# Performance work log

Hardware: AMD Instinct MI355X
Metric: run time of the kernel (lower is better)

The kernel has to match this reference:

```python
import jax, jax.numpy as jnp
import numpy as np

N = 50000   # nodes
E = 800000  # edges
F = 128     # input features
H = 128     # hidden channels
G = 64      # graphs in batch
C = 10      # classes
L_HID = 3   # residual hidden GCN blocks
EPS = 1e-5  # BatchNorm eps


def setup_inputs() -> dict:
    key = jax.random.key(0)
    ks = jax.random.split(key, 10)
    sc = lambda k, s: (jax.random.normal(k, s, jnp.float32) * 0.05)
    x = jax.random.normal(ks[0], (N, F), jnp.float32)
    edge_index = jax.random.randint(ks[1], (2, E), 0, N, dtype=jnp.int32)
    batch = jnp.sort(jax.random.randint(ks[2], (N,), 0, G, dtype=jnp.int32))
    return {
        "x": x, "edge_index": edge_index, "batch": batch,
        # initial GCN block
        "W0": sc(ks[3], (F, H)), "b0": jnp.zeros(H, jnp.float32),
        "g0": jnp.ones(H, jnp.float32), "be0": jnp.zeros(H, jnp.float32),
        # 3 residual GCN blocks (stacked)
        "Wh": sc(ks[4], (L_HID, H, H)), "bh": jnp.zeros((L_HID, H), jnp.float32),
        "gh": jnp.ones((L_HID, H), jnp.float32), "beh": jnp.zeros((L_HID, H), jnp.float32),
        "Rh": sc(ks[5], (L_HID, H, H)),  # residual Linear (no bias)
        # MLP head: Linear(H,H)+ReLU, Linear(H,C)
        "mW1": sc(ks[6], (H, H)), "mb1": jnp.zeros(H, jnp.float32),
        "mW2": sc(ks[7], (H, C)), "mb2": jnp.zeros(C, jnp.float32),
    }


def _gcn_norm(edge_index, n):
    # add self-loops + symmetric normalization, as in PyG GCNConv
    loop = jnp.arange(n, dtype=edge_index.dtype)
    src = jnp.concatenate([edge_index[0], loop])
    dst = jnp.concatenate([edge_index[1], loop])
    deg = jax.ops.segment_sum(jnp.ones_like(dst, jnp.float32), dst, num_segments=n)
    dinv = jnp.where(deg > 0, jax.lax.rsqrt(deg), 0.0)
    coef = dinv[src] * dinv[dst]  # [E+N]
    return src, dst, coef


def _gcn_conv(x, W, b, src, dst, coef, n):
    h = x @ W                                   # [N, H] linear first (PyG order)
    msg = h[src] * coef[:, None]                # gather + normalize  [E+N, H]
    agg = jax.ops.segment_sum(msg, dst, num_segments=n)  # scatter-add [N, H]
    return agg + b


def _bn_relu(h, gamma, beta):
    # BatchNorm1d in eval mode with running_mean=0, running_var=1
    inv = jax.lax.rsqrt(jnp.asarray(1.0 + EPS, h.dtype))
    return jax.nn.relu(h * inv * gamma + beta)  # dropout is identity in eval


def reference(x, edge_index, batch, W0, b0, g0, be0, Wh, bh, gh, beh, Rh, mW1, mb1, mW2, mb2):
    n = x.shape[0]
    src, dst, coef = _gcn_norm(edge_index, n)
    # initial block (no residual)
    h = _bn_relu(_gcn_conv(x, W0, b0, src, dst, coef, n), g0, be0)
    # residual hidden blocks
    for i in range(Wh.shape[0]):
        c = _gcn_conv(h, Wh[i], bh[i], src, dst, coef, n) + h @ Rh[i]
        h = _bn_relu(c, gh[i], beh[i])
    # global max pool over graphs in the batch
    pooled = jax.ops.segment_max(h, batch, num_segments=G)  # [G, H]
    # MLP head
    z = jax.nn.relu(pooled @ mW1 + mb1)
    return z @ mW2 + mb2  # [G, C]
```

## Files before the change

### kernel.cpp

```cpp
#include <hip/hip_runtime.h>
#include <cstdint>
#include <cstddef>

#define NN 50000
#define NE 800000
#define NEPAD (NE + 3 * NN)
#define HID 128
#define NGRAPH 64
#define NCLASS 10
#define LHID 3
#define NREP 8

#define ROWBLK 3125
#define ROWBLK_PAD 3128
#define GEMM_GRID 782
#define FILL_GRID 3125
#define FRONT_DEG 3125
#define FRONT_B 56
#define FRONT_GRID (FRONT_DEG + FRONT_B)

static constexpr float BN_INV = 0.9999950000374996f;

typedef __attribute__((ext_vector_type(8))) __bf16 bf16x8;
typedef __attribute__((ext_vector_type(4))) float floatx4;


__device__ __forceinline__ unsigned int f32_to_bf16_rne(float f) {
    unsigned int u = __float_as_uint(f);
    return (u + 0x7FFFu + ((u >> 16) & 1u)) >> 16;
}
__device__ __forceinline__ float bf16_to_f32(unsigned int h) {
    return __uint_as_float(h << 16);
}
__device__ __forceinline__ void split2(float a, float b, unsigned int& hi,
                                       unsigned int& lo) {
    unsigned int h0 = f32_to_bf16_rne(a), h1 = f32_to_bf16_rne(b);
    unsigned int l0 = f32_to_bf16_rne(a - bf16_to_f32(h0));
    unsigned int l1 = f32_to_bf16_rne(b - bf16_to_f32(h1));
    hi = h0 | (h1 << 16);
    lo = l0 | (l1 << 16);
}


__global__ void k_front(const float* __restrict__ W0, const float* __restrict__ Wh,
                        const float* __restrict__ Rh, unsigned short* __restrict__ bH,
                        unsigned short* __restrict__ bL,
                        const int* __restrict__ ei, int* __restrict__ deg8,
                        int* __restrict__ eslot) {
    const int b = blockIdx.x;
    const int tid = threadIdx.x;
    if (b < FRONT_DEG) {
        int e = b * 256 + tid;
        int d = ei[NE + e];
        int rep = e & (NREP - 1);
        eslot[e] = atomicAdd(&deg8[rep * NN + d], 1);
    } else {
        int cb = b - FRONT_DEG;
        int mat = cb >> 3;
        const float* src = (mat == 0) ? W0
                         : (mat <= 3) ? (Wh + (size_t)(mat - 1) * 16384)
                                      : (Rh + (size_t)(mat - 4) * 16384);
        int u = (cb & 7) * 256 + tid;
        int lane = u & 63;
        int blk = u >> 6;
        int kblk = blk & 3;
        int nb = blk >> 2;
        int n = nb * 16 + (lane & 15);
        int k = kblk * 32 + (lane >> 4) * 8;
        union { unsigned int i[4]; uint4 v; } H, L;
#pragma unroll
        for (int j = 0; j < 4; ++j) {
            float a = src[(size_t)(k + 2 * j) * 128 + n];
            float c = src[(size_t)(k + 2 * j + 1) * 128 + n];
            split2(a, c, H.i[j], L.i[j]);
        }
        size_t base = (size_t)mat * 16384 + (size_t)u * 8;
        *(uint4*)&bH[base] = H.v;
        *(uint4*)&bL[base] = L.v;
    }
}


__global__ void k_scan1(const int* __restrict__ deg8, int* __restrict__ degT,
                        int* __restrict__ degOff, float* __restrict__ dinv,
                        int* __restrict__ bsum) {
    __shared__ int s[256];
    int i = blockIdx.x * 256 + threadIdx.x;
    int dsum = 0;
    if (i < NN) {
        int off[NREP];
#pragma unroll
        for (int r = 0; r < NREP; ++r) {
            off[r] = dsum;
            dsum += deg8[r * NN + i];
        }
#pragma unroll
        for (int r = 0; r < NREP; ++r) degOff[i * NREP + r] = off[r];
        degT[i] = dsum;
        dinv[i] = rsqrtf((float)(dsum + 1));
    }
    s[threadIdx.x] = (dsum + 3) & ~3;
    __syncthreads();
    for (int o = 128; o > 0; o >>= 1) {
        if (threadIdx.x < o) s[threadIdx.x] += s[threadIdx.x + o];
        __syncthreads();
    }
    if (threadIdx.x == 0) bsum[blockIdx.x] = s[0];
}


__global__ void k_scan3(const int* __restrict__ degT, const int* __restrict__ bsum,
                        int* __restrict__ rowptr, int* __restrict__ col,
                        float* __restrict__ cfv) {
    __shared__ int s[256];
    __shared__ int offS;
    const int bid = blockIdx.x;
    s[threadIdx.x] = (threadIdx.x < bid) ? bsum[threadIdx.x] : 0;
    __syncthreads();
    for (int o = 128; o > 0; o >>= 1) {
        if (threadIdx.x < o) s[threadIdx.x] += s[threadIdx.x + o];
        __syncthreads();
    }
    if (threadIdx.x == 0) offS = s[0];
    __syncthreads();
    const int off = offS;
    __syncthreads();
    int i = bid * 256 + threadIdx.x;
    int d = (i < NN) ? degT[i] : 0;
    int v = (d + 3) & ~3;
    s[threadIdx.x] = v;
    __syncthreads();
    for (int o = 1; o < 256; o <<= 1) {
        int tv = (threadIdx.x >= o) ? s[threadIdx.x - o] : 0;
        __syncthreads();
        s[threadIdx.x] += tv;
        __syncthreads();
    }
    if (i < NN) {
        int rp = off + s[threadIdx.x] - v;
        rowptr[i] = rp;
        for (int p = rp + d; p < rp + v; ++p) { col[p] = 0; cfv[p] = 0.f; }
    }
}


template <int NB, bool FILL, bool XA>
__global__ __launch_bounds__(256, 3) void k_gemm_mfma(
    const float* __restrict__ X,
    const unsigned short* __restrict__ Ahi, const unsigned short* __restrict__ Alo,
    const unsigned short* __restrict__ B1hi, const unsigned short* __restrict__ B1lo,
    const unsigned short* __restrict__ B2hi, const unsigned short* __restrict__ B2lo,
    float* __restrict__ C1, float* __restrict__ C2,
    const int* __restrict__ ei, const int* __restrict__ rowptr,
    const int* __restrict__ eslot, const int* __restrict__ degOff,
    const float* __restrict__ dinv, int* __restrict__ col,
    float* __restrict__ cfv) {
    if (FILL && blockIdx.x >= GEMM_GRID) {
        int e = (blockIdx.x - GEMM_GRID) * 256 + threadIdx.x;
        int s = ei[e];
        int d = ei[NE + e];
        int rep = e & (NREP - 1);
        int p = rowptr[d] + degOff[d * NREP + rep] + eslot[e];
        col[p] = s;
        cfv[p] = dinv[s];
        return;
    }
    const int tid = threadIdx.x;
    const int wave = tid >> 6;
    const int lane = tid & 63;
    const int wm = wave & 1;
    const int wn = wave >> 1;
    const int rb0 = blockIdx.x * 4;

    floatx4 acc1[2][4], acc2[2][4];
    floatx4 zero = {0.f, 0.f, 0.f, 0.f};
#pragma unroll
    for (int i = 0; i < 2; ++i)
#pragma unroll
        for (int j = 0; j < 4; ++j) { acc1[i][j] = zero; if (NB == 2) acc2[i][j] = zero; }

#pragma unroll
    for (int kc = 0; kc < 4; ++kc) {
        bf16x8 aH[2], aL[2], bH[4], bL[4];
        if (XA) {
#pragma unroll
            for (int t = 0; t < 2; ++t) {
                int m = (rb0 + wm * 2 + t) * 16 + (lane & 15);
                if (m >= NN) m = NN - 1;
                const float4* p =
                    (const float4*)&X[(size_t)m * 128 + kc * 32 + (lane >> 4) * 8];
                float4 v0 = p[0];
                float4 v1 = p[1];
                float vals[8] = {v0.x, v0.y, v0.z, v0.w, v1.x, v1.y, v1.z, v1.w};
                union { unsigned int i[4]; bf16x8 v; } H, L;
#pragma unroll
                for (int j = 0; j < 4; ++j)
                    split2(vals[2 * j], vals[2 * j + 1], H.i[j], L.i[j]);
                aH[t] = H.v;
                aL[t] = L.v;
            }
        } else {
#pragma unroll
            for (int t = 0; t < 2; ++t) {
                size_t u = ((size_t)(rb0 + wm * 2 + t) * 4 + kc) * 512 + lane * 8;
                aH[t] = *(const bf16x8*)(Ahi + u);
                aL[t] = *(const bf16x8*)(Alo + u);
            }
        }
#pragma unroll
        for (int t = 0; t < 4; ++t)
            bH[t] = *(const bf16x8*)(B1hi + ((size_t)(wn * 4 + t) * 4 + kc) * 512 +
                                     lane * 8);
#pragma unroll
        for (int tm = 0; tm < 2; ++tm)
#pragma unroll
            for (int tn = 0; tn < 4; ++tn)
                acc1[tm][tn] = __builtin_amdgcn_mfma_f32_16x16x32_bf16(
                    aH[tm], bH[tn], acc1[tm][tn], 0, 0, 0);
#pragma unroll
        for (int t = 0; t < 4; ++t)
            bL[t] = *(const bf16x8*)(B1lo + ((size_t)(wn * 4 + t) * 4 + kc) * 512 +
                                     lane * 8);
#pragma unroll
        for (int tm = 0; tm < 2; ++tm)
#pragma unroll
            for (int tn = 0; tn < 4; ++tn)
                acc1[tm][tn] = __builtin_amdgcn_mfma_f32_16x16x32_bf16(
                    aH[tm], bL[tn], acc1[tm][tn], 0, 0, 0);
#pragma unroll
        for (int tm = 0; tm < 2; ++tm)
#pragma unroll
            for (int tn = 0; tn < 4; ++tn)
                acc1[tm][tn] = __builtin_amdgcn_mfma_f32_16x16x32_bf16(
                    aL[tm], bH[tn], acc1[tm][tn], 0, 0, 0);
        if (NB == 2) {
#pragma unroll
            for (int t = 0; t < 4; ++t)
                bH[t] = *(const bf16x8*)(B2hi + ((size_t)(wn * 4 + t) * 4 + kc) * 512 +
                                         lane * 8);
#pragma unroll
            for (int tm = 0; tm < 2; ++tm)
#pragma unroll
                for (int tn = 0; tn < 4; ++tn)
                    acc2[tm][tn] = __builtin_amdgcn_mfma_f32_16x16x32_bf16(
                        aH[tm], bH[tn], acc2[tm][tn], 0, 0, 0);
#pragma unroll
            for (int tm = 0; tm < 2; ++tm)
#pragma unroll
                for (int tn = 0; tn < 4; ++tn)
                    acc2[tm][tn] = __builtin_amdgcn_mfma_f32_16x16x32_bf16(
                        aL[tm], bH[tn], acc2[tm][tn], 0, 0, 0);
#pragma unroll
            for (int t = 0; t < 4; ++t)
                bL[t] = *(const bf16x8*)(B2lo + ((size_t)(wn * 4 + t) * 4 + kc) * 512 +
                                         lane * 8);
#pragma unroll
            for (int tm = 0; tm < 2; ++tm)
#pragma unroll
                for (int tn = 0; tn < 4; ++tn)
                    acc2[tm][tn] = __builtin_amdgcn_mfma_f32_16x16x32_bf16(
                        aH[tm], bL[tn], acc2[tm][tn], 0, 0, 0);
        }
    }

    const int quad = lane >> 4;
    const int col0 = lane & 15;
    const int rowBase = blockIdx.x * 64 + wm * 32;
#pragma unroll
    for (int tm = 0; tm < 2; ++tm) {
#pragma unroll
        for (int tn = 0; tn < 4; ++tn) {
            int c = wn * 64 + tn * 16 + col0;
#pragma unroll
            for (int r = 0; r < 4; ++r) {
                int row = rowBase + tm * 16 + quad * 4 + r;
                if (row < NN) {
                    C1[(size_t)row * 128 + c] = acc1[tm][tn][r];
                    if (NB == 2) C2[(size_t)row * 128 + c] = acc2[tm][tn][r];
                }
            }
        }
    }
}


template <bool RES, bool LAST>
__global__ __launch_bounds__(1024, 8) void k_spmm(
    const float* __restrict__ t, const float* __restrict__ r,
    const int* __restrict__ rowptr, const int* __restrict__ degT,
    const int* __restrict__ col, const float* __restrict__ cfv,
    const float* __restrict__ dinv, const float* __restrict__ bias,
    const float* __restrict__ gamma, const float* __restrict__ beta,
    unsigned short* __restrict__ hHi, unsigned short* __restrict__ hLo,
    const int* __restrict__ batch, float* __restrict__ pooled) {
    __shared__ unsigned short shH[16][136];
    __shared__ unsigned short shL[16][136];
    __shared__ float shP[16][128];
    const int tid = threadIdx.x;
    const int lane = tid & 63;
    const int h = lane >> 5;
    const int f4 = lane & 31;
    const int wv = __builtin_amdgcn_readfirstlane(tid >> 6);
    const int node = blockIdx.x * 16 + wv;

    const int start = __builtin_amdgcn_readfirstlane(rowptr[node]);
    const int cnt4 = __builtin_amdgcn_readfirstlane((degT[node] + 3) >> 2);

    float4 acc = {0.f, 0.f, 0.f, 0.f};
#pragma unroll 4
    for (int q = 0; q < cnt4; ++q) {
        const int4 cs = *(const int4*)(col + start + q * 4);
        const float4 wvv = *(const float4*)(cfv + start + q * 4);
        const int rowA = h ? cs.y : cs.x;
        const int rowB = h ? cs.w : cs.z;
        const float wA = h ? wvv.y : wvv.x;
        const float wB = h ? wvv.w : wvv.z;
        const float4 vA = *(const float4*)&t[(size_t)rowA * 128 + f4 * 4];
        const float4 vB = *(const float4*)&t[(size_t)rowB * 128 + f4 * 4];
        acc.x = fmaf(wA, vA.x, acc.x); acc.y = fmaf(wA, vA.y, acc.y);
        acc.z = fmaf(wA, vA.z, acc.z); acc.w = fmaf(wA, vA.w, acc.w);
        acc.x = fmaf(wB, vB.x, acc.x); acc.y = fmaf(wB, vB.y, acc.y);
        acc.z = fmaf(wB, vB.z, acc.z); acc.w = fmaf(wB, vB.w, acc.w);
    }
    acc.x += __shfl_xor(acc.x, 32);
    acc.y += __shfl_xor(acc.y, 32);
    acc.z += __shfl_xor(acc.z, 32);
    acc.w += __shfl_xor(acc.w, 32);

    const int f0 = f4 * 4;
    float4 o;
    if (h == 0) {
        const float di = dinv[node];
        const float dii = di * di;
        const float4 tv = *(const float4*)&t[(size_t)node * 128 + f0];
        const float4 bv = *(const float4*)&bias[f0];
        const float4 gv = *(const float4*)&gamma[f0];
        const float4 ev = *(const float4*)&beta[f0];
        float4 cc;
        cc.x = di * acc.x + dii * tv.x + bv.x;
        cc.y = di * acc.y + dii * tv.y + bv.y;
        cc.z = di * acc.z + dii * tv.z + bv.z;
        cc.w = di * acc.w + dii * tv.w + bv.w;
        if (RES) {
            const float4 rv = *(const float4*)&r[(size_t)node * 128 + f0];
            cc.x += rv.x; cc.y += rv.y; cc.z += rv.z; cc.w += rv.w;
        }
        o.x = fmaxf(cc.x * (BN_INV * gv.x) + ev.x, 0.f);
        o.y = fmaxf(cc.y * (BN_INV * gv.y) + ev.y, 0.f);
        o.z = fmaxf(cc.z * (BN_INV * gv.z) + ev.z, 0.f);
        o.w = fmaxf(cc.w * (BN_INV * gv.w) + ev.w, 0.f);
    }

    if (LAST) {
        bool uni = (batch[blockIdx.x * 16] == batch[blockIdx.x * 16 + 15]);
        if (uni) {
            if (h == 0) *(float4*)&shP[wv][f0] = o;
            __syncthreads();
            if (wv == 0) {
                float a = shP[0][2 * lane], b = shP[0][2 * lane + 1];
#pragma unroll
                for (int w = 1; w < 16; ++w) {
                    a = fmaxf(a, shP[w][2 * lane]);
                    b = fmaxf(b, shP[w][2 * lane + 1]);
                }
                int g = batch[blockIdx.x * 16];
                atomicMax((unsigned int*)&pooled[g * 128 + 2 * lane],
                          __float_as_uint(a));
                atomicMax((unsigned int*)&pooled[g * 128 + 2 * lane + 1],
                          __float_as_uint(b));
            }
        } else if (h == 0) {
            int g = batch[node];
            atomicMax((unsigned int*)&pooled[g * 128 + f0], __float_as_uint(o.x));
            atomicMax((unsigned int*)&pooled[g * 128 + f0 + 1], __float_as_uint(o.y));
            atomicMax((unsigned int*)&pooled[g * 128 + f0 + 2], __float_as_uint(o.z));
            atomicMax((unsigned int*)&pooled[g * 128 + f0 + 3], __float_as_uint(o.w));
        }
        return;
    }

    if (h == 0) {
        unsigned int H0, L0, H1, L1;
        split2(o.x, o.y, H0, L0);
        split2(o.z, o.w, H1, L1);
        ((unsigned int*)&shH[wv][0])[f4 * 2] = H0;
        ((unsigned int*)&shH[wv][0])[f4 * 2 + 1] = H1;
        ((unsigned int*)&shL[wv][0])[f4 * 2] = L0;
        ((unsigned int*)&shL[wv][0])[f4 * 2 + 1] = L1;
    }
    __syncthreads();

    const int u = tid >> 6;
    const int l = tid & 63;
    const int m = l & 15;
    const int kg = l >> 4;
    if (u < 4) {
        uint4 H4 = *(const uint4*)&shH[m][u * 32 + kg * 8];
        ((uint4*)hHi)[((size_t)blockIdx.x * 4 + u) * 64 + l] = H4;
    } else if (u < 8) {
        int uu = u - 4;
        uint4 L4 = *(const uint4*)&shL[m][uu * 32 + kg * 8];
        ((uint4*)hLo)[((size_t)blockIdx.x * 4 + uu) * 64 + l] = L4;
    }
}


__global__ void k_head(const float* __restrict__ pooled, const float* __restrict__ mW1,
                       const float* __restrict__ mb1, const float* __restrict__ mW2,
                       const float* __restrict__ mb2, float* __restrict__ out) {
    __shared__ float p[128];
    __shared__ float z[128];
    int g = blockIdx.x;
    int j = threadIdx.x;
    p[j] = pooled[g * 128 + j];
    __syncthreads();
    float a = mb1[j];
#pragma unroll 8
    for (int k = 0; k < 128; ++k) a += p[k] * mW1[k * 128 + j];
    z[j] = fmaxf(a, 0.f);
    __syncthreads();
    if (j < NCLASS) {
        float o = mb2[j];
#pragma unroll 8
        for (int k = 0; k < 128; ++k) o += z[k] * mW2[k * NCLASS + j];
        out[g * NCLASS + j] = o;
    }
}


extern "C" void kernel_launch(void* const* d_in, const int* in_sizes, int n_in,
                              void* d_out, int out_size, void* d_ws, size_t ws_size,
                              hipStream_t stream) {
    const float* x   = (const float*)d_in[0];
    const int*   ei  = (const int*)d_in[1];
    const int* batch = (const int*)d_in[2];
    const float* W0  = (const float*)d_in[3];
    const float* b0  = (const float*)d_in[4];
    const float* g0  = (const float*)d_in[5];
    const float* be0 = (const float*)d_in[6];
    const float* Wh  = (const float*)d_in[7];
    const float* bh  = (const float*)d_in[8];
    const float* gh  = (const float*)d_in[9];
    const float* beh = (const float*)d_in[10];
    const float* Rh  = (const float*)d_in[11];
    const float* mW1 = (const float*)d_in[12];
    const float* mb1 = (const float*)d_in[13];
    const float* mW2 = (const float*)d_in[14];
    const float* mb2 = (const float*)d_in[15];
    float* out = (float*)d_out;

    char* ws = (char*)d_ws;
    size_t off = 0;
    auto alloc = [&](size_t bytes) -> void* {
        void* p = ws + off;
        off += (bytes + 255) & ~(size_t)255;
        return p;
    };
    int*   deg8   = (int*)alloc((size_t)NREP * NN * 4);
    float* pooled = (float*)alloc((size_t)NGRAPH * HID * 4);
    size_t zspan = (size_t)((char*)pooled - (char*)deg8) + (size_t)NGRAPH * HID * 4;
    int*   degT   = (int*)alloc((size_t)NN * 4);
    int*   degOff = (int*)alloc((size_t)NN * NREP * 4);
    int*   rowptr = (int*)alloc((size_t)NN * 4);
    float* dinv   = (float*)alloc((size_t)NN * 4);
    int*   bsum   = (int*)alloc(256 * 4);
    int*   eslot  = (int*)alloc((size_t)NE * 4);
    int*   col    = (int*)alloc((size_t)NEPAD * 4);
    float* cfv    = (float*)alloc((size_t)NEPAD * 4);
    float* t      = (float*)alloc((size_t)NN * HID * 4);
    float* rbuf   = (float*)alloc((size_t)NN * HID * 4);
    const size_t ASZ = (size_t)ROWBLK_PAD * 4 * 512;
    unsigned short* hH0 = (unsigned short*)alloc(ASZ * 2);
    unsigned short* hL0 = (unsigned short*)alloc(ASZ * 2);
    unsigned short* hH1 = (unsigned short*)alloc(ASZ * 2);
    unsigned short* hL1 = (unsigned short*)alloc(ASZ * 2);
    unsigned short* bH = (unsigned short*)alloc((size_t)7 * 16384 * 2);
    unsigned short* bL = (unsigned short*)alloc((size_t)7 * 16384 * 2);

    hipMemsetAsync(deg8, 0, zspan, stream);

    k_front<<<FRONT_GRID, 256, 0, stream>>>(W0, Wh, Rh, bH, bL, ei, deg8, eslot);
    k_scan1<<<(NN + 255) / 256, 256, 0, stream>>>(deg8, degT, degOff, dinv, bsum);
    k_scan3<<<(NN + 255) / 256, 256, 0, stream>>>(degT, bsum, rowptr, col, cfv);

    k_gemm_mfma<1, true, true><<<GEMM_GRID + FILL_GRID, 256, 0, stream>>>(
        x, nullptr, nullptr, bH, bL, nullptr, nullptr, t, nullptr,
        ei, rowptr, eslot, degOff, dinv, col, cfv);

    const int spmmGrid = NN / 16;
    k_spmm<false, false><<<spmmGrid, 1024, 0, stream>>>(
        t, nullptr, rowptr, degT, col, cfv, dinv, b0, g0, be0, hH0, hL0,
        nullptr, nullptr);

    unsigned short* hh[2] = {hH0, hH1};
    unsigned short* hl[2] = {hL0, hL1};
    int cur = 0;
    for (int i = 0; i < LHID; ++i) {
        unsigned short* ih = hh[cur];
        unsigned short* il = hl[cur];
        unsigned short* oh = hh[cur ^ 1];
        unsigned short* ol = hl[cur ^ 1];
        const unsigned short* w1H = bH + (size_t)(1 + i) * 16384;
        const unsigned short* w1L = bL + (size_t)(1 + i) * 16384;
        const unsigned short* w2H = bH + (size_t)(4 + i) * 16384;
        const unsigned short* w2L = bL + (size_t)(4 + i) * 16384;
        k_gemm_mfma<2, false, false><<<GEMM_GRID, 256, 0, stream>>>(
            nullptr, ih, il, w1H, w1L, w2H, w2L, t, rbuf,
            nullptr, nullptr, nullptr, nullptr, nullptr, nullptr, nullptr);
        if (i < LHID - 1)
            k_spmm<true, false><<<spmmGrid, 1024, 0, stream>>>(
                t, rbuf, rowptr, degT, col, cfv, dinv, bh + i * HID, gh + i * HID,
                beh + i * HID, oh, ol, nullptr, nullptr);
        else
            k_spmm<true, true><<<spmmGrid, 1024, 0, stream>>>(
                t, rbuf, rowptr, degT, col, cfv, dinv, bh + i * HID, gh + i * HID,
                beh + i * HID, nullptr, nullptr, batch, pooled);
        cur ^= 1;
    }

    k_head<<<NGRAPH, 128, 0, stream>>>(pooled, mW1, mb1, mW2, mb2, out);
}
```

Baseline: 502.2 us.

## Fuse next layer's dual GEMM into SpMM epilogue, removing separate GEMM launches

The SpMM kernel now multiplies its 16 freshly aggregated node rows (held in shared memory as bf16 hi/lo splits) by the next layer's W and residual R matrices using MFMA, and writes the fp32 t and r outputs directly. This removes the three standalone GEMM kernels and the write and re-read of the intermediate bf16 hidden state. It uses ping-pong t/r buffers instead. The cost is extra MFMA work and weight-fragment loads inside each SpMM block, with weights read from global memory per wave rather than staged.

```diff
diff --git a/kernel.cpp b/kernel.cpp
--- a/kernel.cpp
+++ b/kernel.cpp
@@ -291,7 +291,9 @@
     const int* __restrict__ col, const float* __restrict__ cfv,
     const float* __restrict__ dinv, const float* __restrict__ bias,
     const float* __restrict__ gamma, const float* __restrict__ beta,
-    unsigned short* __restrict__ hHi, unsigned short* __restrict__ hLo,
+    const unsigned short* __restrict__ w1H, const unsigned short* __restrict__ w1L,
+    const unsigned short* __restrict__ w2H, const unsigned short* __restrict__ w2L,
+    float* __restrict__ tOut, float* __restrict__ rOut,
     const int* __restrict__ batch, float* __restrict__ pooled) {
     __shared__ unsigned short shH[16][136];
     __shared__ unsigned short shL[16][136];
@@ -390,18 +392,30 @@
     }
     __syncthreads();
 
-    const int u = tid >> 6;
-    const int l = tid & 63;
-    const int m = l & 15;
-    const int kg = l >> 4;
-    if (u < 4) {
-        uint4 H4 = *(const uint4*)&shH[m][u * 32 + kg * 8];
-        ((uint4*)hHi)[((size_t)blockIdx.x * 4 + u) * 64 + l] = H4;
-    } else if (u < 8) {
-        int uu = u - 4;
-        uint4 L4 = *(const uint4*)&shL[m][uu * 32 + kg * 8];
-        ((uint4*)hLo)[((size_t)blockIdx.x * 4 + uu) * 64 + l] = L4;
-    }
+    const int w = tid >> 6;
+    const int mat = w >> 3;
+    const int nb = w & 7;
+    const unsigned short* BH = mat ? w2H : w1H;
+    const unsigned short* BL = mat ? w2L : w1L;
+    float* outp = mat ? rOut : tOut;
+    floatx4 accG = {0.f, 0.f, 0.f, 0.f};
+#pragma unroll
+    for (int kc = 0; kc < 4; ++kc) {
+        const int ao = kc * 32 + (lane >> 4) * 8;
+        bf16x8 aH = *(const bf16x8*)&shH[lane & 15][ao];
+        bf16x8 aL = *(const bf16x8*)&shL[lane & 15][ao];
+        bf16x8 bHv = *(const bf16x8*)(BH + ((size_t)nb * 4 + kc) * 512 + lane * 8);
+        bf16x8 bLv = *(const bf16x8*)(BL + ((size_t)nb * 4 + kc) * 512 + lane * 8);
+        accG = __builtin_amdgcn_mfma_f32_16x16x32_bf16(aH, bHv, accG, 0, 0, 0);
+        accG = __builtin_amdgcn_mfma_f32_16x16x32_bf16(aH, bLv, accG, 0, 0, 0);
+        accG = __builtin_amdgcn_mfma_f32_16x16x32_bf16(aL, bHv, accG, 0, 0, 0);
+    }
+    const int quad = lane >> 4;
+    const int c0 = nb * 16 + (lane & 15);
+    const int row0 = blockIdx.x * 16 + quad * 4;
+#pragma unroll
+    for (int rr = 0; rr < 4; ++rr)
+        outp[(size_t)(row0 + rr) * 128 + c0] = accG[rr];
 }
 
 
@@ -467,13 +481,10 @@
     int*   eslot  = (int*)alloc((size_t)NE * 4);
     int*   col    = (int*)alloc((size_t)NEPAD * 4);
     float* cfv    = (float*)alloc((size_t)NEPAD * 4);
-    float* t      = (float*)alloc((size_t)NN * HID * 4);
-    float* rbuf   = (float*)alloc((size_t)NN * HID * 4);
-    const size_t ASZ = (size_t)ROWBLK_PAD * 4 * 512;
-    unsigned short* hH0 = (unsigned short*)alloc(ASZ * 2);
-    unsigned short* hL0 = (unsigned short*)alloc(ASZ * 2);
-    unsigned short* hH1 = (unsigned short*)alloc(ASZ * 2);
-    unsigned short* hL1 = (unsigned short*)alloc(ASZ * 2);
+    float* tA     = (float*)alloc((size_t)NN * HID * 4);
+    float* tB     = (float*)alloc((size_t)NN * HID * 4);
+    float* rA     = (float*)alloc((size_t)NN * HID * 4);
+    float* rB     = (float*)alloc((size_t)NN * HID * 4);
     unsigned short* bH = (unsigned short*)alloc((size_t)7 * 16384 * 2);
     unsigned short* bL = (unsigned short*)alloc((size_t)7 * 16384 * 2);
 
@@ -484,39 +495,36 @@
     k_scan3<<<(NN + 255) / 256, 256, 0, stream>>>(degT, bsum, rowptr, col, cfv);
 
     k_gemm_mfma<1, true, true><<<GEMM_GRID + FILL_GRID, 256, 0, stream>>>(
-        x, nullptr, nullptr, bH, bL, nullptr, nullptr, t, nullptr,
+        x, nullptr, nullptr, bH, bL, nullptr, nullptr, tA, nullptr,
         ei, rowptr, eslot, degOff, dinv, col, cfv);
 
     const int spmmGrid = NN / 16;
+
     k_spmm<false, false><<<spmmGrid, 1024, 0, stream>>>(
-        t, nullptr, rowptr, degT, col, cfv, dinv, b0, g0, be0, hH0, hL0,
-        nullptr, nullptr);
-
-    unsigned short* hh[2] = {hH0, hH1};
-    unsigned short* hl[2] = {hL0, hL1};
-    int cur = 0;
-    for (int i = 0; i < LHID; ++i) {
-        unsigned short* ih = hh[cur];
-        unsigned short* il = hl[cur];
-        unsigned short* oh = hh[cur ^ 1];
-        unsigned short* ol = hl[cur ^ 1];
-        const unsigned short* w1H = bH + (size_t)(1 + i) * 16384;
-        const unsigned short* w1L = bL + (size_t)(1 + i) * 16384;
-        const unsigned short* w2H = bH + (size_t)(4 + i) * 16384;
-        const unsigned short* w2L = bL + (size_t)(4 + i) * 16384;
-        k_gemm_mfma<2, false, false><<<GEMM_GRID, 256, 0, stream>>>(
-            nullptr, ih, il, w1H, w1L, w2H, w2L, t, rbuf,
-            nullptr, nullptr, nullptr, nullptr, nullptr, nullptr, nullptr);
-        if (i < LHID - 1)
-            k_spmm<true, false><<<spmmGrid, 1024, 0, stream>>>(
-                t, rbuf, rowptr, degT, col, cfv, dinv, bh + i * HID, gh + i * HID,
-                beh + i * HID, oh, ol, nullptr, nullptr);
-        else
-            k_spmm<true, true><<<spmmGrid, 1024, 0, stream>>>(
-                t, rbuf, rowptr, degT, col, cfv, dinv, bh + i * HID, gh + i * HID,
-                beh + i * HID, nullptr, nullptr, batch, pooled);
-        cur ^= 1;
-    }
+        tA, nullptr, rowptr, degT, col, cfv, dinv, b0, g0, be0,
+        bH + (size_t)1 * 16384, bL + (size_t)1 * 16384,
+        bH + (size_t)4 * 16384, bL + (size_t)4 * 16384,
+        tB, rB, nullptr, nullptr);
+
+    k_spmm<true, false><<<spmmGrid, 1024, 0, stream>>>(
+        tB, rB, rowptr, degT, col, cfv, dinv, bh + 0 * HID, gh + 0 * HID,
+        beh + 0 * HID,
+        bH + (size_t)2 * 16384, bL + (size_t)2 * 16384,
+        bH + (size_t)5 * 16384, bL + (size_t)5 * 16384,
+        tA, rA, nullptr, nullptr);
+
+    k_spmm<true, false><<<spmmGrid, 1024, 0, stream>>>(
+        tA, rA, rowptr, degT, col, cfv, dinv, bh + 1 * HID, gh + 1 * HID,
+        beh + 1 * HID,
+        bH + (size_t)3 * 16384, bL + (size_t)3 * 16384,
+        bH + (size_t)6 * 16384, bL + (size_t)6 * 16384,
+        tB, rB, nullptr, nullptr);
+
+    k_spmm<true, true><<<spmmGrid, 1024, 0, stream>>>(
+        tB, rB, rowptr, degT, col, cfv, dinv, bh + 2 * HID, gh + 2 * HID,
+        beh + 2 * HID,
+        nullptr, nullptr, nullptr, nullptr,
+        nullptr, nullptr, batch, pooled);
 
     k_head<<<NGRAPH, 128, 0, stream>>>(pooled, mW1, mb1, mW2, mb2, out);
 }
```

After: 474.6 us. 1.06x faster.

## Slice feature matrix into 16-column panels and pack edge metadata for SpMM

Applied to the files above, without the earlier changes.

The GEMM now writes its output in eight column-sliced panels of 16 floats per node, and the SpMM grid is multiplied by 8 so each block aggregates one 16-feature slice. With 16 edges per wave in parallel, each gather is a 64-byte contiguous row piece. Edge column index and source degree are packed into one int, with the coefficient recomputed by rsqrt, which replaces the separate col and cfv arrays. The intent is to keep each slice's gather working set small enough to stay in cache. In exchange, metadata is re-read eight times and more blocks are launched. The hidden-state buffers are also reorganised: one h buffer with ping-ponged t and r buffers.

```diff
diff --git a/kernel.cpp b/kernel.cpp
--- a/kernel.cpp
+++ b/kernel.cpp
@@ -18,6 +18,9 @@
 #define FRONT_DEG 3125
 #define FRONT_B 56
 #define FRONT_GRID (FRONT_DEG + FRONT_B)
+
+#define SPMM_GRID (NN / 16 * 8)
+#define SLICE_STRIDE ((size_t)NN * 16)
 
 static constexpr float BN_INV = 0.9999950000374996f;
 
@@ -110,8 +113,7 @@
 
 
 __global__ void k_scan3(const int* __restrict__ degT, const int* __restrict__ bsum,
-                        int* __restrict__ rowptr, int* __restrict__ col,
-                        float* __restrict__ cfv) {
+                        int* __restrict__ rowptr, int* __restrict__ meta) {
     __shared__ int s[256];
     __shared__ int offS;
     const int bid = blockIdx.x;
@@ -139,7 +141,7 @@
     if (i < NN) {
         int rp = off + s[threadIdx.x] - v;
         rowptr[i] = rp;
-        for (int p = rp + d; p < rp + v; ++p) { col[p] = 0; cfv[p] = 0.f; }
+        for (int p = rp + d; p < rp + v; ++p) meta[p] = (int)0x80000000u;
     }
 }
 
@@ -153,16 +155,14 @@
     float* __restrict__ C1, float* __restrict__ C2,
     const int* __restrict__ ei, const int* __restrict__ rowptr,
     const int* __restrict__ eslot, const int* __restrict__ degOff,
-    const float* __restrict__ dinv, int* __restrict__ col,
-    float* __restrict__ cfv) {
+    const int* __restrict__ degT, int* __restrict__ meta) {
     if (FILL && blockIdx.x >= GEMM_GRID) {
         int e = (blockIdx.x - GEMM_GRID) * 256 + threadIdx.x;
         int s = ei[e];
         int d = ei[NE + e];
         int rep = e & (NREP - 1);
         int p = rowptr[d] + degOff[d * NREP + rep] + eslot[e];
-        col[p] = s;
-        cfv[p] = dinv[s];
+        meta[p] = s | (degT[s] << 17);
         return;
     }
     const int tid = threadIdx.x;
@@ -271,12 +271,13 @@
 #pragma unroll
         for (int tn = 0; tn < 4; ++tn) {
             int c = wn * 64 + tn * 16 + col0;
+            size_t sb = (size_t)(c >> 4) * SLICE_STRIDE + (size_t)(c & 15);
 #pragma unroll
             for (int r = 0; r < 4; ++r) {
                 int row = rowBase + tm * 16 + quad * 4 + r;
                 if (row < NN) {
-                    C1[(size_t)row * 128 + c] = acc1[tm][tn][r];
-                    if (NB == 2) C2[(size_t)row * 128 + c] = acc2[tm][tn][r];
+                    C1[sb + (size_t)row * 16] = acc1[tm][tn][r];
+                    if (NB == 2) C2[sb + (size_t)row * 16] = acc2[tm][tn][r];
                 }
             }
         }
@@ -285,91 +286,89 @@
 
 
 template <bool RES, bool LAST>
-__global__ __launch_bounds__(1024, 8) void k_spmm(
+__global__ __launch_bounds__(1024, 2) void k_spmm(
     const float* __restrict__ t, const float* __restrict__ r,
     const int* __restrict__ rowptr, const int* __restrict__ degT,
-    const int* __restrict__ col, const float* __restrict__ cfv,
-    const float* __restrict__ dinv, const float* __restrict__ bias,
-    const float* __restrict__ gamma, const float* __restrict__ beta,
+    const int* __restrict__ meta, const float* __restrict__ dinv,
+    const float* __restrict__ bias, const float* __restrict__ gamma,
+    const float* __restrict__ beta,
     unsigned short* __restrict__ hHi, unsigned short* __restrict__ hLo,
     const int* __restrict__ batch, float* __restrict__ pooled) {
-    __shared__ unsigned short shH[16][136];
-    __shared__ unsigned short shL[16][136];
-    __shared__ float shP[16][128];
+    __shared__ float sh[16][20];
     const int tid = threadIdx.x;
     const int lane = tid & 63;
-    const int h = lane >> 5;
-    const int f4 = lane & 31;
+    const int e = lane >> 2;
+    const int c = lane & 3;
+    const int s = blockIdx.x & 7;
+    const int nb = blockIdx.x >> 3;
     const int wv = __builtin_amdgcn_readfirstlane(tid >> 6);
-    const int node = blockIdx.x * 16 + wv;
+    const int node = nb * 16 + wv;
+    const float* ts = t + (size_t)s * SLICE_STRIDE;
 
     const int start = __builtin_amdgcn_readfirstlane(rowptr[node]);
-    const int cnt4 = __builtin_amdgcn_readfirstlane((degT[node] + 3) >> 2);
+    const int pcnt = __builtin_amdgcn_readfirstlane((degT[node] + 3) & ~3);
 
     float4 acc = {0.f, 0.f, 0.f, 0.f};
-#pragma unroll 4
-    for (int q = 0; q < cnt4; ++q) {
-        const int4 cs = *(const int4*)(col + start + q * 4);
-        const float4 wvv = *(const float4*)(cfv + start + q * 4);
-        const int rowA = h ? cs.y : cs.x;
-        const int rowB = h ? cs.w : cs.z;
-        const float wA = h ? wvv.y : wvv.x;
-        const float wB = h ? wvv.w : wvv.z;
-        const float4 vA = *(const float4*)&t[(size_t)rowA * 128 + f4 * 4];
-        const float4 vB = *(const float4*)&t[(size_t)rowB * 128 + f4 * 4];
-        acc.x = fmaf(wA, vA.x, acc.x); acc.y = fmaf(wA, vA.y, acc.y);
-        acc.z = fmaf(wA, vA.z, acc.z); acc.w = fmaf(wA, vA.w, acc.w);
-        acc.x = fmaf(wB, vB.x, acc.x); acc.y = fmaf(wB, vB.y, acc.y);
-        acc.z = fmaf(wB, vB.z, acc.z); acc.w = fmaf(wB, vB.w, acc.w);
-    }
-    acc.x += __shfl_xor(acc.x, 32);
-    acc.y += __shfl_xor(acc.y, 32);
-    acc.z += __shfl_xor(acc.z, 32);
-    acc.w += __shfl_xor(acc.w, 32);
-
-    const int f0 = f4 * 4;
+#pragma unroll 2
+    for (int q0 = 0; q0 < pcnt; q0 += 16) {
+        const int idx = q0 + e;
+        const bool act = idx < pcnt;
+        const unsigned int mv =
+            (unsigned int)meta[act ? (start + idx) : start];
+        const int ci = (int)(mv & 0x1FFFFu);
+        float w = rsqrtf((float)((mv >> 17) + 1u));
+        w = (act && (int)mv >= 0) ? w : 0.f;
+        const float4 tv = *(const float4*)&ts[(size_t)ci * 16 + c * 4];
+        acc.x = fmaf(w, tv.x, acc.x);
+        acc.y = fmaf(w, tv.y, acc.y);
+        acc.z = fmaf(w, tv.z, acc.z);
+        acc.w = fmaf(w, tv.w, acc.w);
+    }
+#pragma unroll
+    for (int mk = 4; mk <= 32; mk <<= 1) {
+        acc.x += __shfl_xor(acc.x, mk);
+        acc.y += __shfl_xor(acc.y, mk);
+        acc.z += __shfl_xor(acc.z, mk);
+        acc.w += __shfl_xor(acc.w, mk);
+    }
+
+    const float di = dinv[node];
+    const float dii = di * di;
+    const int f0 = s * 16 + c * 4;
+    const float4 tvs = *(const float4*)&ts[(size_t)node * 16 + c * 4];
+    const float4 bv = *(const float4*)&bias[f0];
+    const float4 gv = *(const float4*)&gamma[f0];
+    const float4 ev = *(const float4*)&beta[f0];
+    float4 cc;
+    cc.x = di * acc.x + dii * tvs.x + bv.x;
+    cc.y = di * acc.y + dii * tvs.y + bv.y;
+    cc.z = di * acc.z + dii * tvs.z + bv.z;
+    cc.w = di * acc.w + dii * tvs.w + bv.w;
+    if (RES) {
+        const float4 rv = *(const float4*)&r[(size_t)s * SLICE_STRIDE +
+                                             (size_t)node * 16 + c * 4];
+        cc.x += rv.x; cc.y += rv.y; cc.z += rv.z; cc.w += rv.w;
+    }
     float4 o;
-    if (h == 0) {
-        const float di = dinv[node];
-        const float dii = di * di;
-        const float4 tv = *(const float4*)&t[(size_t)node * 128 + f0];
-        const float4 bv = *(const float4*)&bias[f0];
-        const float4 gv = *(const float4*)&gamma[f0];
-        const float4 ev = *(const float4*)&beta[f0];
-        float4 cc;
-        cc.x = di * acc.x + dii * tv.x + bv.x;
-        cc.y = di * acc.y + dii * tv.y + bv.y;
-        cc.z = di * acc.z + dii * tv.z + bv.z;
-        cc.w = di * acc.w + dii * tv.w + bv.w;
-        if (RES) {
-            const float4 rv = *(const float4*)&r[(size_t)node * 128 + f0];
-            cc.x += rv.x; cc.y += rv.y; cc.z += rv.z; cc.w += rv.w;
-        }
-        o.x = fmaxf(cc.x * (BN_INV * gv.x) + ev.x, 0.f);
-        o.y = fmaxf(cc.y * (BN_INV * gv.y) + ev.y, 0.f);
-        o.z = fmaxf(cc.z * (BN_INV * gv.z) + ev.z, 0.f);
-        o.w = fmaxf(cc.w * (BN_INV * gv.w) + ev.w, 0.f);
-    }
+    o.x = fmaxf(cc.x * (BN_INV * gv.x) + ev.x, 0.f);
+    o.y = fmaxf(cc.y * (BN_INV * gv.y) + ev.y, 0.f);
+    o.z = fmaxf(cc.z * (BN_INV * gv.z) + ev.z, 0.f);
+    o.w = fmaxf(cc.w * (BN_INV * gv.w) + ev.w, 0.f);
 
     if (LAST) {
-        bool uni = (batch[blockIdx.x * 16] == batch[blockIdx.x * 16 + 15]);
+        bool uni = (batch[nb * 16] == batch[nb * 16 + 15]);
         if (uni) {
-            if (h == 0) *(float4*)&shP[wv][f0] = o;
+            if (e == 0) *(float4*)&sh[wv][c * 4] = o;
             __syncthreads();
-            if (wv == 0) {
-                float a = shP[0][2 * lane], b = shP[0][2 * lane + 1];
-#pragma unroll
-                for (int w = 1; w < 16; ++w) {
-                    a = fmaxf(a, shP[w][2 * lane]);
-                    b = fmaxf(b, shP[w][2 * lane + 1]);
-                }
-                int g = batch[blockIdx.x * 16];
-                atomicMax((unsigned int*)&pooled[g * 128 + 2 * lane],
+            if (tid < 16) {
+                float a = sh[0][tid];
+#pragma unroll
+                for (int w2 = 1; w2 < 16; ++w2) a = fmaxf(a, sh[w2][tid]);
+                int g = batch[nb * 16];
+                atomicMax((unsigned int*)&pooled[g * 128 + s * 16 + tid],
                           __float_as_uint(a));
-                atomicMax((unsigned int*)&pooled[g * 128 + 2 * lane + 1],
-                          __float_as_uint(b));
             }
-        } else if (h == 0) {
+        } else if (e == 0) {
             int g = batch[node];
             atomicMax((unsigned int*)&pooled[g * 128 + f0], __float_as_uint(o.x));
             atomicMax((unsigned int*)&pooled[g * 128 + f0 + 1], __float_as_uint(o.y));
@@ -379,28 +378,22 @@
         return;
     }
 
-    if (h == 0) {
-        unsigned int H0, L0, H1, L1;
-        split2(o.x, o.y, H0, L0);
-        split2(o.z, o.w, H1, L1);
-        ((unsigned int*)&shH[wv][0])[f4 * 2] = H0;
-        ((unsigned int*)&shH[wv][0])[f4 * 2 + 1] = H1;
-        ((unsigned int*)&shL[wv][0])[f4 * 2] = L0;
-        ((unsigned int*)&shL[wv][0])[f4 * 2 + 1] = L1;
-    }
-    __syncthreads();
-
-    const int u = tid >> 6;
-    const int l = tid & 63;
-    const int m = l & 15;
-    const int kg = l >> 4;
-    if (u < 4) {
-        uint4 H4 = *(const uint4*)&shH[m][u * 32 + kg * 8];
-        ((uint4*)hHi)[((size_t)blockIdx.x * 4 + u) * 64 + l] = H4;
-    } else if (u < 8) {
-        int uu = u - 4;
-        uint4 L4 = *(const uint4*)&shL[m][uu * 32 + kg * 8];
-        ((uint4*)hLo)[((size_t)blockIdx.x * 4 + uu) * 64 + l] = L4;
+    if (e == 0) *(float4*)&sh[wv][c * 4] = o;
+    __syncthreads();
+    if (tid < 32) {
+        const int mm = tid & 15;
+        const int k8l = tid >> 4;
+        float v[8];
+#pragma unroll
+        for (int jj = 0; jj < 8; ++jj) v[jj] = sh[mm][k8l * 8 + jj];
+        union { unsigned int i[4]; uint4 u; } H, L;
+#pragma unroll
+        for (int jj = 0; jj < 4; ++jj)
+            split2(v[2 * jj], v[2 * jj + 1], H.i[jj], L.i[jj]);
+        const size_t uidx =
+            (size_t)(nb * 4 + (s >> 1)) * 64 + (size_t)((s & 1) * 32 + tid);
+        ((uint4*)hHi)[uidx] = H.u;
+        ((uint4*)hLo)[uidx] = L.u;
     }
 }
 
@@ -465,15 +458,14 @@
     float* dinv   = (float*)alloc((size_t)NN * 4);
     int*   bsum   = (int*)alloc(256 * 4);
     int*   eslot  = (int*)alloc((size_t)NE * 4);
-    int*   col    = (int*)alloc((size_t)NEPAD * 4);
-    float* cfv    = (float*)alloc((size_t)NEPAD * 4);
-    float* t      = (float*)alloc((size_t)NN * HID * 4);
-    float* rbuf   = (float*)alloc((size_t)NN * HID * 4);
+    int*   meta   = (int*)alloc((size_t)(NEPAD + 64) * 4);
+    float* tA     = (float*)alloc((size_t)NN * HID * 4);
+    float* tB     = (float*)alloc((size_t)NN * HID * 4);
+    float* rA     = (float*)alloc((size_t)NN * HID * 4);
+    float* rB     = (float*)alloc((size_t)NN * HID * 4);
     const size_t ASZ = (size_t)ROWBLK_PAD * 4 * 512;
-    unsigned short* hH0 = (unsigned short*)alloc(ASZ * 2);
-    unsigned short* hL0 = (unsigned short*)alloc(ASZ * 2);
-    unsigned short* hH1 = (unsigned short*)alloc(ASZ * 2);
-    unsigned short* hL1 = (unsigned short*)alloc(ASZ * 2);
+    unsigned short* hH = (unsigned short*)alloc(ASZ * 2);
+    unsigned short* hL = (unsigned short*)alloc(ASZ * 2);
     unsigned short* bH = (unsigned short*)alloc((size_t)7 * 16384 * 2);
     unsigned short* bL = (unsigned short*)alloc((size_t)7 * 16384 * 2);
 
@@ -481,41 +473,34 @@
 
     k_front<<<FRONT_GRID, 256, 0, stream>>>(W0, Wh, Rh, bH, bL, ei, deg8, eslot);
     k_scan1<<<(NN + 255) / 256, 256, 0, stream>>>(deg8, degT, degOff, dinv, bsum);
-    k_scan3<<<(NN + 255) / 256, 256, 0, stream>>>(degT, bsum, rowptr, col, cfv);
+    k_scan3<<<(NN + 255) / 256, 256, 0, stream>>>(degT, bsum, rowptr, meta);
 
     k_gemm_mfma<1, true, true><<<GEMM_GRID + FILL_GRID, 256, 0, stream>>>(
-        x, nullptr, nullptr, bH, bL, nullptr, nullptr, t, nullptr,
-        ei, rowptr, eslot, degOff, dinv, col, cfv);
-
-    const int spmmGrid = NN / 16;
-    k_spmm<false, false><<<spmmGrid, 1024, 0, stream>>>(
-        t, nullptr, rowptr, degT, col, cfv, dinv, b0, g0, be0, hH0, hL0,
+        x, nullptr, nullptr, bH, bL, nullptr, nullptr, tA, nullptr,
+        ei, rowptr, eslot, degOff, degT, meta);
+
+    k_spmm<false, false><<<SPMM_GRID, 1024, 0, stream>>>(
+        tA, nullptr, rowptr, degT, meta, dinv, b0, g0, be0, hH, hL,
         nullptr, nullptr);
 
-    unsigned short* hh[2] = {hH0, hH1};
-    unsigned short* hl[2] = {hL0, hL1};
-    int cur = 0;
+    float* tP[2] = {tB, tA};
+    float* rP[2] = {rB, rA};
     for (int i = 0; i < LHID; ++i) {
-        unsigned short* ih = hh[cur];
-        unsigned short* il = hl[cur];
-        unsigned short* oh = hh[cur ^ 1];
-        unsigned short* ol = hl[cur ^ 1];
-        const unsigned short* w1H = bH + (size_t)(1 + i) * 16384;
-        const unsigned short* w1L = bL + (size_t)(1 + i) * 16384;
-        const unsigned short* w2H = bH + (size_t)(4 + i) * 16384;
-        const unsigned short* w2L = bL + (size_t)(4 + i) * 16384;
+        float* tN = tP[i & 1];
+        float* rN = rP[i & 1];
         k_gemm_mfma<2, false, false><<<GEMM_GRID, 256, 0, stream>>>(
-            nullptr, ih, il, w1H, w1L, w2H, w2L, t, rbuf,
-            nullptr, nullptr, nullptr, nullptr, nullptr, nullptr, nullptr);
+            nullptr, hH, hL,
+            bH + (size_t)(1 + i) * 16384, bL + (size_t)(1 + i) * 16384,
+            bH + (size_t)(4 + i) * 16384, bL + (size_t)(4 + i) * 16384,
+            tN, rN, nullptr, nullptr, nullptr, nullptr, nullptr, nullptr);
         if (i < LHID - 1)
-            k_spmm<true, false><<<spmmGrid, 1024, 0, stream>>>(
-                t, rbuf, rowptr, degT, col, cfv, dinv, bh + i * HID, gh + i * HID,
-                beh + i * HID, oh, ol, nullptr, nullptr);
+            k_spmm<true, false><<<SPMM_GRID, 1024, 0, stream>>>(
+                tN, rN, rowptr, degT, meta, dinv, bh + i * HID, gh + i * HID,
+                beh + i * HID, hH, hL, nullptr, nullptr);
         else
-            k_spmm<true, true><<<spmmGrid, 1024, 0, stream>>>(
-                t, rbuf, rowptr, degT, col, cfv, dinv, bh + i * HID, gh + i * HID,
+            k_spmm<true, true><<<SPMM_GRID, 1024, 0, stream>>>(
+                tN, rN, rowptr, degT, meta, dinv, bh + i * HID, gh + i * HID,
                 beh + i * HID, nullptr, nullptr, batch, pooled);
-        cur ^= 1;
     }
 
     k_head<<<NGRAPH, 128, 0, stream>>>(pooled, mW1, mb1, mW2, mb2, out);
```

Result: slower. 776.0 us (+54.5%).
